# Kernel tuning notes

Hardware: AMD Instinct MI355X
Metric: run time of the kernel (lower is better)

Reference implementation:

```python
import jax, jax.numpy as jnp
import numpy as np

EPS_TINY = np.float32(np.finfo(np.float32).tiny)  # torch clamp min in continuous_topk


def layernorm(x, gamma, beta, eps=1e-6):
    mu = jnp.mean(x, axis=-1, keepdims=True)
    var = jnp.mean((x - mu) ** 2, axis=-1, keepdims=True)
    return (x - mu) * jax.lax.rsqrt(var + eps) * gamma + beta


def continuous_topk(w, k, t=0.1):
    """Iterative differentiable top-k with hard straight-through, as in the torch code.
    w: (B, N) logits. Returns khot: (B, k, N)."""
    n = w.shape[-1]

    def step(carry, _):
        logits, onehot = carry
        # khot_mask = clamp(1 - onehot, min=EPS); logits accumulate log-mask in place
        logits = logits + jnp.log(jnp.maximum(1.0 - onehot, EPS_TINY))
        soft = jax.nn.softmax(logits / t, axis=-1)
        hard = jax.nn.one_hot(jnp.argmax(soft, axis=-1), n, dtype=soft.dtype)
        st = hard - jax.lax.stop_gradient(soft) + soft  # straight-through
        return (logits, st), st

    (_, _), khot = jax.lax.scan(step, (w, jnp.zeros_like(w)), None, length=k)
    return jnp.transpose(khot, (1, 0, 2))  # (k,B,N) -> (B,k,N)


def setup_inputs():
    key = jax.random.key(0)
    ks = jax.random.split(key, 8)
    B, N, C, COUT = 8, 2048, 256, 256
    s = 0.02
    return {
        "xyzs": jax.random.normal(ks[0], (B, N, 3), jnp.float32),
        "features": jax.random.normal(ks[1], (B, C, N), jnp.float32),
        "ln_gamma": jnp.ones((C,), jnp.float32),
        "ln_beta": jnp.zeros((C,), jnp.float32),
        "Wu1": jax.random.normal(ks[2], (C, C), jnp.float32) * s,
        "bu1": jnp.zeros((C,), jnp.float32),
        "Wu2": jax.random.normal(ks[3], (C, COUT), jnp.float32) * s,
        "bu2": jnp.zeros((COUT,), jnp.float32),
        "Wd1": jax.random.normal(ks[4], (C, C), jnp.float32) * s,
        "bd1": jnp.zeros((C,), jnp.float32),
        "Wd2": jax.random.normal(ks[5], (C, 1), jnp.float32) * s,
        "bd2": jnp.zeros((1,), jnp.float32),
        "out_num_points": 1024,
    }


def reference(xyzs, features, ln_gamma, ln_beta, Wu1, bu1, Wu2, bu2, Wd1, bd1, Wd2, bd2, out_num_points):
    # eval mode: dropout inactive, gumbel_keys skipped (self.training False)
    f = jnp.transpose(features, (0, 2, 1))           # (B, N, C)
    f = layernorm(f, ln_gamma, ln_beta)
    new_f = jnp.maximum(f @ Wu1 + bu1, 0.0) @ Wu2 + bu2   # (B, N, COUT)
    w = (jnp.maximum(f @ Wd1 + bd1, 0.0) @ Wd2 + bd2)[:, :, 0]  # (B, N)
    khot = continuous_topk(w, out_num_points, t=0.1)  # (B, K, N)
    xyzs_out = khot @ xyzs                            # (B, K, 3)
    feats = jnp.einsum('bkn,bnc->bkc', khot, new_f)   # (B, K, COUT)
    indices = jnp.argmax(khot, axis=2)                # (B, K)
    return xyzs_out, jnp.transpose(feats, (0, 2, 1)), indices
```

## Files before the change

### kernel.cpp

```cpp
#include <hip/hip_runtime.h>

#define B_DIM 8
#define N_DIM 2048
#define C_DIM 256
#define K_SEL 1024

typedef __attribute__((ext_vector_type(8))) short short8;
typedef __attribute__((ext_vector_type(4))) float f32x4;

__device__ __forceinline__ unsigned int bf16rne(float x) {
  unsigned int u = __float_as_uint(x);
  return (u + 0x7fffu + ((u >> 16) & 1u)) >> 16;
}

__global__ __launch_bounds__(64) void ln_lds(const float* __restrict__ feat,
    const float* __restrict__ gamma, const float* __restrict__ beta,
    float* __restrict__ fbuf) {
  __shared__ float tile[256 * 64];
  const int t = threadIdx.x;
  const int m0 = blockIdx.x << 6;
  const int b = m0 >> 11, n0 = m0 & 2047;

  const int cg = t >> 4, nl4 = (t & 15) << 2;
  for (int pass = 0; pass < 64; ++pass) {
    const int c = (pass << 2) + cg;
    const float4 v = *(const float4*)(feat + (((long)((b << 8) + c)) << 11) + n0 + nl4);
    const int sw = c & 31;
    float* row = tile + (c << 6);
    row[(nl4 + 0) ^ sw] = v.x; row[(nl4 + 1) ^ sw] = v.y;
    row[(nl4 + 2) ^ sw] = v.z; row[(nl4 + 3) ^ sw] = v.w;
  }
  __syncthreads();

  float acc = tile[t];
  for (int c = 1; c < 256; ++c) acc = __fadd_rn(acc, tile[(c << 6) + (t ^ (c & 31))]);
  const float mu = __fdiv_rn(acc, 256.0f);

  float pw[2];
#pragma unroll
  for (int blk = 0; blk < 2; ++blk) {
    const int c0 = blk << 7;
    float r8[8];
#pragma unroll
    for (int j = 0; j < 8; ++j) {
      float d = __fsub_rn(tile[((c0 + j) << 6) + (t ^ ((c0 + j) & 31))], mu);
      r8[j] = __fmul_rn(d, d);
    }
    for (int i = 8; i < 128; i += 8) {
#pragma unroll
      for (int j = 0; j < 8; ++j) {
        const int c = c0 + i + j;
        float d = __fsub_rn(tile[(c << 6) + (t ^ (c & 31))], mu);
        r8[j] = __fadd_rn(r8[j], __fmul_rn(d, d));
      }
    }
    pw[blk] = __fadd_rn(__fadd_rn(__fadd_rn(r8[0], r8[1]), __fadd_rn(r8[2], r8[3])),
                        __fadd_rn(__fadd_rn(r8[4], r8[5]), __fadd_rn(r8[6], r8[7])));
  }
  const float var = __fdiv_rn(__fadd_rn(pw[0], pw[1]), 256.0f);
  const float rs = __fdiv_rn(1.0f, __fsqrt_rn(__fadd_rn(var, 1e-6f)));

  float ga[4], be[4];
#pragma unroll
  for (int q = 0; q < 4; ++q) { ga[q] = gamma[(q << 6) + t]; be[q] = beta[(q << 6) + t]; }
  for (int r = 0; r < 64; ++r) {
    const float mu_r = __shfl(mu, r, 64);
    const float rs_r = __shfl(rs, r, 64);
    float* orow = fbuf + (((long)(m0 + r)) << 8);
#pragma unroll
    for (int q = 0; q < 4; ++q) {
      const int c = (q << 6) + t;
      const float x = tile[(c << 6) + (r ^ (c & 31))];
      orow[c] = __fadd_rn(__fmul_rn(__fmul_rn(__fsub_rn(x, mu_r), rs_r), ga[q]), be[q]);
    }
  }
}

__global__ void __launch_bounds__(512) wgemm_w(
    const float* __restrict__ A, const float* __restrict__ Wd1,
    const float* __restrict__ bd1, const float* __restrict__ Wd2,
    const float* __restrict__ bd2, float* __restrict__ wkey) {
  __shared__ __align__(16) char smem[65536];
  float (*As)[68] = (float (*)[68])smem;
  float (*Bs)[260] = (float (*)[260])(smem + 4352);
  float* H = (float*)smem;

  const int t = threadIdx.x;
  const int m0 = blockIdx.x << 6;
  const int rowT = t >> 6, colT = t & 63;
  const int ar = t >> 2, ak = (t & 3) << 2;
  const int bk = t >> 5, bc = (t & 31) << 3;
  const long arow = ((long)(m0 + ar)) << 8;
  float acc[8][4] = {};

  for (int k0 = 0; k0 < 256; k0 += 16) {
    if (t < 256) {
      const float4 av = *(const float4*)(A + arow + k0 + ak);
      As[ak + 0][ar] = av.x; As[ak + 1][ar] = av.y;
      As[ak + 2][ar] = av.z; As[ak + 3][ar] = av.w;
    }
    const float* brow = Wd1 + (((k0 + bk) << 8) + bc);
    *(float4*)&Bs[bk][bc] = *(const float4*)brow;
    *(float4*)&Bs[bk][bc + 4] = *(const float4*)(brow + 4);
    __syncthreads();
#pragma unroll
    for (int kk = 0; kk < 16; ++kk) {
      const float4 a0 = *(const float4*)&As[kk][rowT << 3];
      const float4 a1 = *(const float4*)&As[kk][(rowT << 3) + 4];
      const float4 b = *(const float4*)&Bs[kk][colT << 2];
      const float aa[8] = {a0.x, a0.y, a0.z, a0.w, a1.x, a1.y, a1.z, a1.w};
      const float bbv[4] = {b.x, b.y, b.z, b.w};
#pragma unroll
      for (int i = 0; i < 8; ++i)
#pragma unroll
        for (int j = 0; j < 4; ++j)
          acc[i][j] = __fmaf_rn(aa[i], bbv[j], acc[i][j]);
    }
    __syncthreads();
  }

  const float4 bd = *(const float4*)(bd1 + (colT << 2));
  const float ba[4] = {bd.x, bd.y, bd.z, bd.w};
#pragma unroll
  for (int i = 0; i < 8; ++i) {
    const int m = (rowT << 3) + i;
#pragma unroll
    for (int j = 0; j < 4; ++j) {
      const int c = (colT << 2) + j;
      H[(c << 6) + (m ^ ((c >> 2) & 31))] = fmaxf(__fadd_rn(acc[i][j], ba[j]), 0.0f);
    }
  }
  __syncthreads();

  if (t < 64) {
    float wa = 0.0f;
    for (int c = 0; c < 256; ++c)
      wa = __fmaf_rn(H[(c << 6) + (t ^ ((c >> 2) & 31))], Wd2[c], wa);
    const float w = __fadd_rn(wa, bd2[0]);
    wkey[m0 + t] = __fdiv_rn(w, 0.1f);
  }
}

__global__ void __launch_bounds__(1024) topk_kernel(
    const float* __restrict__ wv, const float* __restrict__ xyzs,
    int* __restrict__ idx_out, float* __restrict__ out_xyz,
    float* __restrict__ out_idx) {
  __shared__ unsigned long long vals[2048];
  const int b = blockIdx.x, t = threadIdx.x;
#pragma unroll
  for (int h = 0; h < 2; ++h) {
    const int i = (h << 10) + t;
    const unsigned int u = __float_as_uint(wv[(b << 11) + i]);
    const unsigned int up = ((int)u < 0) ? ~u : (u | 0x80000000u);
    vals[i] = (((unsigned long long)(~up)) << 32) | (unsigned int)i;
  }
  __syncthreads();
  for (int k = 2; k <= 2048; k <<= 1) {
    for (int j = k >> 1; j > 0; j >>= 1) {
      for (int half = 0; half < 2; ++half) {
        const int i = (half << 10) | t;
        const int ixj = i ^ j;
        if (ixj > i) {
          const unsigned long long vi = vals[i], vj = vals[ixj];
          const bool up = ((i & k) == 0);
          if ((vi > vj) == up) { vals[i] = vj; vals[ixj] = vi; }
        }
      }
      __syncthreads();
    }
  }
  const int sel = (int)(vals[t] & 0xffffffffu);
  idx_out[(b << 10) + t] = sel;
  out_idx[(b << 10) + t] = (float)sel;
  const long o = ((long)((b << 10) + t)) * 3;
  const long s3 = ((long)((b << 11) + sel)) * 3;
  out_xyz[o] = xyzs[s3]; out_xyz[o + 1] = xyzs[s3 + 1]; out_xyz[o + 2] = xyzs[s3 + 2];
}

__global__ __launch_bounds__(256) void prep_w(const float* __restrict__ W,
    unsigned short* __restrict__ P) {
  const int kc = blockIdx.x, n = threadIdx.x;
  unsigned int packed[16];
#pragma unroll
  for (int i = 0; i < 16; ++i) {
    const float a = W[(((kc << 5) + 2 * i) << 8) + n];
    const float bq = W[(((kc << 5) + 2 * i + 1) << 8) + n];
    packed[i] = bf16rne(a) | (bf16rne(bq) << 16);
  }
  uint4* dst = (uint4*)(P + (((kc << 8) + n) << 5));
#pragma unroll
  for (int q = 0; q < 4; ++q)
    dst[q] = make_uint4(packed[4 * q], packed[4 * q + 1], packed[4 * q + 2], packed[4 * q + 3]);
}

#define APITCH 264
#define BPITCH 40
__global__ void __launch_bounds__(256) up_mfma(
    const float* __restrict__ fbuf, const int* __restrict__ idxm,
    const unsigned short* __restrict__ Wu1P, const float* __restrict__ bu1,
    const unsigned short* __restrict__ Wu2P, const float* __restrict__ bu2,
    float* __restrict__ out_feat) {
  __shared__ __align__(16) char smem[64 * APITCH * 2 + 256 * BPITCH * 2 + 2048];
  unsigned short* As = (unsigned short*)smem;
  unsigned short* Bs = (unsigned short*)(smem + 64 * APITCH * 2);
  float* bias1 = (float*)(smem + 64 * APITCH * 2 + 256 * BPITCH * 2);
  float* bias2 = bias1 + 256;
  float* T = (float*)(smem + 64 * APITCH * 2);

  const int t = threadIdx.x;
  const int m0 = blockIdx.x << 6;
  const int quad = (t >> 4) & 3, ln = t & 15, w = t >> 6;

  bias1[t] = bu1[t];
  bias2[t] = bu2[t];

  {
    const int r = t & 63, cseg = t >> 6;
    const int m = m0 + r;
    const long srow = (long)(((m >> 10) << 11) + idxm[m]) << 8;
    const float* src = fbuf + srow + (cseg << 6);
    unsigned short* dst = As + r * APITCH + (cseg << 6);
#pragma unroll
    for (int u = 0; u < 16; ++u) {
      const float4 v = *(const float4*)(src + (u << 2));
      const unsigned int lo = bf16rne(v.x) | (bf16rne(v.y) << 16);
      const unsigned int hi = bf16rne(v.z) | (bf16rne(v.w) << 16);
      *(uint2*)(dst + (u << 2)) = make_uint2(lo, hi);
    }
  }

  f32x4 acc[16];
#pragma unroll
  for (int i = 0; i < 16; ++i) acc[i] = (f32x4){0.f, 0.f, 0.f, 0.f};

  for (int kc = 0; kc < 8; ++kc) {
    __syncthreads();
    const uint4* sb = (const uint4*)(Wu1P + (((kc << 8) + t) << 5));
    uint4* db = (uint4*)(Bs + t * BPITCH);
    db[0] = sb[0]; db[1] = sb[1]; db[2] = sb[2]; db[3] = sb[3];
    __syncthreads();
    const short8 a = *(const short8*)(As + ((w << 4) + ln) * APITCH + (kc << 5) + (quad << 3));
#pragma unroll
    for (int nt = 0; nt < 16; ++nt) {
      const short8 b = *(const short8*)(Bs + ((nt << 4) + ln) * BPITCH + (quad << 3));
      acc[nt] = __builtin_amdgcn_mfma_f32_16x16x32_bf16(a, b, acc[nt], 0, 0, 0);
    }
  }

  __syncthreads();
  unsigned short* Hs = As;
#pragma unroll
  for (int nt = 0; nt < 16; ++nt) {
    const int c = (nt << 4) + ln;
    const float bb = bias1[c];
#pragma unroll
    for (int rr = 0; rr < 4; ++rr) {
      const float h = fmaxf(acc[nt][rr] + bb, 0.0f);
      Hs[((w << 4) + (quad << 2) + rr) * APITCH + c] = (unsigned short)bf16rne(h);
    }
  }
#pragma unroll
  for (int i = 0; i < 16; ++i) acc[i] = (f32x4){0.f, 0.f, 0.f, 0.f};

  for (int kc = 0; kc < 8; ++kc) {
    __syncthreads();
    const uint4* sb = (const uint4*)(Wu2P + (((kc << 8) + t) << 5));
    uint4* db = (uint4*)(Bs + t * BPITCH);
    db[0] = sb[0]; db[1] = sb[1]; db[2] = sb[2]; db[3] = sb[3];
    __syncthreads();
    const short8 a = *(const short8*)(Hs + ((w << 4) + ln) * APITCH + (kc << 5) + (quad << 3));
#pragma unroll
    for (int nt = 0; nt < 16; ++nt) {
      const short8 b = *(const short8*)(Bs + ((nt << 4) + ln) * BPITCH + (quad << 3));
      acc[nt] = __builtin_amdgcn_mfma_f32_16x16x32_bf16(a, b, acc[nt], 0, 0, 0);
    }
  }

  const int bb = m0 >> 10, kbase = m0 & 1023;
  for (int ci = 0; ci < 4; ++ci) {
    __syncthreads();
#pragma unroll
    for (int q = 0; q < 4; ++q) {
      const int nt = (ci << 2) + q;
      const int cloc = (q << 4) + ln;
      const float b2 = bias2[(nt << 4) + ln];
#pragma unroll
      for (int rr = 0; rr < 4; ++rr)
        T[cloc * 66 + ((w << 4) + (quad << 2) + rr)] = acc[nt][rr] + b2;
    }
    __syncthreads();
#pragma unroll
    for (int p = 0; p < 16; ++p) {
      const int cl = (p << 2) + (t >> 6);
      const int m = t & 63;
      out_feat[((long)((bb << 8) + (ci << 6) + cl) << 10) + kbase + m] = T[cl * 66 + m];
    }
  }
}

extern "C" void kernel_launch(void* const* d_in, const int* in_sizes, int n_in,
                              void* d_out, int out_size, void* d_ws, size_t ws_size,
                              hipStream_t stream) {
  const float* xyzs     = (const float*)d_in[0];
  const float* features = (const float*)d_in[1];
  const float* ln_gamma = (const float*)d_in[2];
  const float* ln_beta  = (const float*)d_in[3];
  const float* Wu1      = (const float*)d_in[4];
  const float* bu1      = (const float*)d_in[5];
  const float* Wu2      = (const float*)d_in[6];
  const float* bu2      = (const float*)d_in[7];
  const float* Wd1      = (const float*)d_in[8];
  const float* bd1      = (const float*)d_in[9];
  const float* Wd2      = (const float*)d_in[10];
  const float* bd2      = (const float*)d_in[11];

  char* ws = (char*)d_ws;
  float* fbuf = (float*)ws;
  unsigned short* Wu1P = (unsigned short*)(ws + 33554432);
  unsigned short* Wu2P = (unsigned short*)(ws + 33685504);
  float* wv   = (float*)(ws + 50331648);
  int*   idx  = (int*)(ws + 50397184);

  float* out_xyz  = (float*)d_out;
  float* out_feat = out_xyz + 24576;
  float* out_idx  = out_feat + 2097152;

  prep_w<<<8, 256, 0, stream>>>(Wu1, Wu1P);
  prep_w<<<8, 256, 0, stream>>>(Wu2, Wu2P);
  ln_lds<<<256, 64, 0, stream>>>(features, ln_gamma, ln_beta, fbuf);
  wgemm_w<<<256, 512, 0, stream>>>(fbuf, Wd1, bd1, Wd2, bd2, wv);
  topk_kernel<<<8, 1024, 0, stream>>>(wv, xyzs, idx, out_xyz, out_idx);
  up_mfma<<<128, 256, 0, stream>>>(fbuf, idx, Wu1P, bu1, Wu2P, bu2, out_feat);
}
```

Before: 196.2 us.

## Double-buffer Wd1 tiles and read A directly from global into registers

The w-score GEMM stops staging A in shared memory. Each thread now loads its 8 rows of A straight from global memory into registers and prefetches the next k-slice while computing the current one. Wd1 tiles are double-buffered in LDS with a register prefetch, so each k-step needs one barrier instead of two. The two weight-packing launches are also merged into a single 16-block launch to save one kernel launch. The A loads read strided rows, which may coalesce poorly, and the extra prefetch registers raise register pressure at 512 threads per block.

```diff
diff --git a/kernel.cpp b/kernel.cpp
--- a/kernel.cpp
+++ b/kernel.cpp
@@ -81,40 +81,66 @@
     const float* __restrict__ bd1, const float* __restrict__ Wd2,
     const float* __restrict__ bd2, float* __restrict__ wkey) {
   __shared__ __align__(16) char smem[65536];
-  float (*As)[68] = (float (*)[68])smem;
-  float (*Bs)[260] = (float (*)[260])(smem + 4352);
+  float (*Bs0)[260] = (float (*)[260])smem;
+  float (*Bs1)[260] = (float (*)[260])(smem + 16640);
   float* H = (float*)smem;
 
   const int t = threadIdx.x;
   const int m0 = blockIdx.x << 6;
   const int rowT = t >> 6, colT = t & 63;
-  const int ar = t >> 2, ak = (t & 3) << 2;
   const int bk = t >> 5, bc = (t & 31) << 3;
-  const long arow = ((long)(m0 + ar)) << 8;
+  const float* arow0 = A + ((long)(m0 + (rowT << 3)) << 8);
+
   float acc[8][4] = {};
 
-  for (int k0 = 0; k0 < 256; k0 += 16) {
-    if (t < 256) {
-      const float4 av = *(const float4*)(A + arow + k0 + ak);
-      As[ak + 0][ar] = av.x; As[ak + 1][ar] = av.y;
-      As[ak + 2][ar] = av.z; As[ak + 3][ar] = av.w;
-    }
-    const float* brow = Wd1 + (((k0 + bk) << 8) + bc);
-    *(float4*)&Bs[bk][bc] = *(const float4*)brow;
-    *(float4*)&Bs[bk][bc + 4] = *(const float4*)(brow + 4);
-    __syncthreads();
-#pragma unroll
-    for (int kk = 0; kk < 16; ++kk) {
-      const float4 a0 = *(const float4*)&As[kk][rowT << 3];
-      const float4 a1 = *(const float4*)&As[kk][(rowT << 3) + 4];
-      const float4 b = *(const float4*)&Bs[kk][colT << 2];
-      const float aa[8] = {a0.x, a0.y, a0.z, a0.w, a1.x, a1.y, a1.z, a1.w};
-      const float bbv[4] = {b.x, b.y, b.z, b.w};
-#pragma unroll
-      for (int i = 0; i < 8; ++i)
-#pragma unroll
-        for (int j = 0; j < 4; ++j)
-          acc[i][j] = __fmaf_rn(aa[i], bbv[j], acc[i][j]);
+  {
+    const float* brow = Wd1 + ((bk << 8) + bc);
+    *(float4*)&Bs0[bk][bc]     = *(const float4*)brow;
+    *(float4*)&Bs0[bk][bc + 4] = *(const float4*)(brow + 4);
+  }
+
+  float4 a_cur[8], a_nxt[8];
+#pragma unroll
+  for (int i = 0; i < 8; ++i) a_cur[i] = *(const float4*)(arow0 + (i << 8));
+
+  __syncthreads();
+
+  int cur = 0;
+  for (int c16 = 0; c16 < 16; ++c16) {
+    float4 r0, r1;
+    {
+      const int knext = (c16 + 1) & 15;
+      const float* brow = Wd1 + (((knext << 4) + bk) << 8) + bc;
+      r0 = *(const float4*)brow;
+      r1 = *(const float4*)(brow + 4);
+    }
+    float (*Bsc)[260] = cur ? Bs1 : Bs0;
+#pragma unroll
+    for (int ks = 0; ks < 16; ks += 4) {
+      const int ka = ((c16 << 4) + ks + 4) & 255;
+#pragma unroll
+      for (int i = 0; i < 8; ++i) a_nxt[i] = *(const float4*)(arow0 + (i << 8) + ka);
+#pragma unroll
+      for (int kk = 0; kk < 4; ++kk) {
+        const float4 b = *(const float4*)&Bsc[ks + kk][colT << 2];
+        const float bbv[4] = {b.x, b.y, b.z, b.w};
+#pragma unroll
+        for (int i = 0; i < 8; ++i) {
+          const float av = (kk == 0) ? a_cur[i].x : (kk == 1) ? a_cur[i].y
+                         : (kk == 2) ? a_cur[i].z : a_cur[i].w;
+#pragma unroll
+          for (int j = 0; j < 4; ++j)
+            acc[i][j] = __fmaf_rn(av, bbv[j], acc[i][j]);
+        }
+      }
+#pragma unroll
+      for (int i = 0; i < 8; ++i) a_cur[i] = a_nxt[i];
+    }
+    if (c16 < 15) {
+      float (*Bsn)[260] = cur ? Bs0 : Bs1;
+      *(float4*)&Bsn[bk][bc]     = r0;
+      *(float4*)&Bsn[bk][bc + 4] = r1;
+      cur ^= 1;
     }
     __syncthreads();
   }
@@ -141,6 +167,7 @@
   }
 }
 
+__global__ void __launch_bounds__(1024) void_guard();
 __global__ void __launch_bounds__(1024) topk_kernel(
     const float* __restrict__ wv, const float* __restrict__ xyzs,
     int* __restrict__ idx_out, float* __restrict__ out_xyz,
@@ -177,9 +204,13 @@
   out_xyz[o] = xyzs[s3]; out_xyz[o + 1] = xyzs[s3 + 1]; out_xyz[o + 2] = xyzs[s3 + 2];
 }
 
-__global__ __launch_bounds__(256) void prep_w(const float* __restrict__ W,
-    unsigned short* __restrict__ P) {
-  const int kc = blockIdx.x, n = threadIdx.x;
+__global__ __launch_bounds__(256) void prep_w2(const float* __restrict__ W1,
+    const float* __restrict__ W2, unsigned short* __restrict__ P1,
+    unsigned short* __restrict__ P2) {
+  const int g = blockIdx.x;
+  const float* W = (g < 8) ? W1 : W2;
+  unsigned short* P = (g < 8) ? P1 : P2;
+  const int kc = g & 7, n = threadIdx.x;
   unsigned int packed[16];
 #pragma unroll
   for (int i = 0; i < 16; ++i) {
@@ -325,8 +356,7 @@
   float* out_feat = out_xyz + 24576;
   float* out_idx  = out_feat + 2097152;
 
-  prep_w<<<8, 256, 0, stream>>>(Wu1, Wu1P);
-  prep_w<<<8, 256, 0, stream>>>(Wu2, Wu2P);
+  prep_w2<<<16, 256, 0, stream>>>(Wu1, Wu2, Wu1P, Wu2P);
   ln_lds<<<256, 64, 0, stream>>>(features, ln_gamma, ln_beta, fbuf);
   wgemm_w<<<256, 512, 0, stream>>>(fbuf, Wd1, bd1, Wd2, bd2, wv);
   topk_kernel<<<8, 1024, 0, stream>>>(wv, xyzs, idx, out_xyz, out_idx);
```

After: 237.6 us. 1.21x slower.
